# Kernel tuning notes

Hardware: AMD Instinct MI355X
Metric: run time of the kernel (lower is better)

Reference implementation:

```python
import jax, jax.numpy as jnp
import numpy as np
from jax import lax

C_IN, C_KEY, C_VAL = 1024, 256, 512

def conv3x3(x, w, b):
    # x: [B,C_in,H,W], w: [C_out,C_in,3,3] -> SAME padding, stride 1
    y = lax.conv_general_dilated(x, w, window_strides=(1, 1), padding='SAME',
                                 dimension_numbers=('NCHW', 'OIHW', 'NCHW'))
    return y + b[None, :, None, None]

def setup_inputs() -> dict:
    key = jax.random.key(0)
    ks = jax.random.split(key, 10)
    B, H, W = 16, 32, 32
    conv_std = 0.01  # matches torch init.normal_(std=0.01)
    inp = {
        'src_temp': jax.random.normal(ks[0], (B, C_IN, H, W), jnp.float32),
        'src_search': jax.random.normal(ks[1], (B, C_IN, H, W), jnp.float32),
        'wk_m': jax.random.normal(ks[2], (C_KEY, C_IN, 3, 3), jnp.float32) * conv_std,
        'bk_m': jnp.zeros((C_KEY,), jnp.float32),
        'wv_m': jax.random.normal(ks[3], (C_VAL, C_IN, 3, 3), jnp.float32) * conv_std,
        'bv_m': jnp.zeros((C_VAL,), jnp.float32),
        'wk_q': jax.random.normal(ks[4], (C_KEY, C_IN, 3, 3), jnp.float32) * conv_std,
        'bk_q': jnp.zeros((C_KEY,), jnp.float32),
        'wv_q': jax.random.normal(ks[5], (C_VAL, C_IN, 3, 3), jnp.float32) * conv_std,
        'bv_q': jnp.zeros((C_VAL,), jnp.float32),
    }
    return inp

def reference(src_temp, src_search, wk_m, bk_m, wv_m, bv_m, wk_q, bk_q, wv_q, bv_q):
    # key/value projections
    m_key = conv3x3(src_temp, wk_m, bk_m)      # [B, Ck, H, W]
    m_value = conv3x3(src_temp, wv_m, bv_m)    # [B, Cv, H, W]
    q_key = conv3x3(src_search, wk_q, bk_q)    # [B, Ck, H, W]
    q_value = conv3x3(src_search, wv_q, bv_q)  # [B, Cv, H, W]

    B, Ck, H, W = m_key.shape
    Cv = m_value.shape[1]
    HW = H * W

    mk = m_key.reshape(B, Ck, HW)   # [B, Ck, HW_m]
    qk = q_key.reshape(B, Ck, HW)   # [B, Ck, HW_q]
    # scores: [B, HW_m, HW_q]
    w = jnp.einsum('bcm,bcq->bmq', mk, qk) / jnp.sqrt(jnp.float32(Ck))
    w = jax.nn.softmax(w, axis=1)   # normalize over memory locations

    mv = m_value.reshape(B, Cv, HW)            # [B, Cv, HW_m]
    mem_info = jnp.einsum('bcm,bmq->bcq', mv, w).reshape(B, Cv, H, W)
    return jnp.concatenate([mem_info, q_value], axis=1)  # [B, 2*Cv, H, W]
```

## Files before the change

### kernel.cpp

```cpp
#include <hip/hip_runtime.h>
#include <stdint.h>

typedef __bf16 bf16;
typedef __bf16 bf16x8 __attribute__((ext_vector_type(8)));
typedef float  f32x4  __attribute__((ext_vector_type(4)));
typedef unsigned int u32;

#define OFF_A16HI 0ull
#define OFF_A16LO 37879808ull
#define OFF_A8HI  0ull
#define OFF_A8LO  18939904ull
#define OFF_W1HI  75759616ull
#define OFF_W1LO  89915392ull
#define OFF_W0HI  37879808ull
#define OFF_W0LO  52035584ull
#define OFF_MKEYT 67108864ull
#define OFF_MVAL  83886080ull
#define OFF_QKEYT 117440512ull
#define OFF_WATTN 0ull

__device__ __forceinline__ void split(float v, bf16& h, bf16& l) {
    h = (bf16)v;
    l = (bf16)(v - (float)h);
}

__device__ __forceinline__ u32 packsplit(float v) {
    bf16 h = (bf16)v;
    bf16 l = (bf16)(v - (float)h);
    unsigned short hu = __builtin_bit_cast(unsigned short, h);
    unsigned short lu = __builtin_bit_cast(unsigned short, l);
    return (u32)hu | ((u32)lu << 16);
}

__device__ __forceinline__ void deint4(const uint4 v, uint2& h, uint2& l) {
    h.x = (v.x & 0xffffu) | (v.y << 16);
    h.y = (v.z & 0xffffu) | (v.w << 16);
    l.x = (v.x >> 16) | (v.y & 0xffff0000u);
    l.y = (v.z >> 16) | (v.w & 0xffff0000u);
}

__global__ __launch_bounds__(256) void k_wt(const float* __restrict__ wk,
                                            const float* __restrict__ wv,
                                            bf16* __restrict__ Wh, bf16* __restrict__ Wl) {
    size_t id = (size_t)blockIdx.x * 256 + threadIdx.x;
    int e = (int)(id & 7);
    size_t t = id >> 3;
    int mm = (int)(t % 96); t /= 96;
    int coff = (int)(t & 3); t >>= 2;
    int cch = (int)(t & 31); t >>= 5;
    int r = (int)(t % 9);
    int mt = (int)(t / 9);
    int m = mt * 96 + mm;
    int c = cch * 32 + coff * 8 + e;
    float v = (m < 256) ? wk[((size_t)m * 1024 + c) * 9 + r]
                        : wv[((size_t)(m - 256) * 1024 + c) * 9 + r];
    bf16 h, l;
    split(v, h, l);
    Wh[id] = h; Wl[id] = l;
}

__global__ __launch_bounds__(256) void k_zero(bf16* __restrict__ A) {
    int id = blockIdx.x * 256 + threadIdx.x;
    int oct = id & 127;
    int t = id >> 7;
    int pos = t % 132; t /= 132;
    int yy, xx;
    if (pos < 34)       { yy = 0;  xx = pos; }
    else if (pos < 68)  { yy = 33; xx = pos - 34; }
    else if (pos < 100) { yy = pos - 68 + 1;  xx = 0; }
    else                { yy = pos - 100 + 1; xx = 33; }
    size_t off = (((size_t)t * 1156) + yy * 34 + xx) * 1024 + (size_t)oct * 8;
    *(uint4*)(A + off) = make_uint4(0u, 0u, 0u, 0u);
}

__global__ __launch_bounds__(256) void k_transpose(const float* __restrict__ src,
                                                   bf16* __restrict__ Ah, bf16* __restrict__ Al) {
    int pt = blockIdx.x, ct = blockIdx.y, bl = blockIdx.z;
    __shared__ float tile[64][68];
    int t = threadIdx.x;
    #pragma unroll
    for (int k = 0; k < 4; ++k) {
        int idx = t + 256 * k;
        int c = idx >> 4, f4 = idx & 15;
        float4 v = *(const float4*)(src + ((size_t)bl * 1024 + ct * 64 + c) * 1024 + pt * 64 + f4 * 4);
        *(float4*)&tile[c][f4 * 4] = v;
    }
    __syncthreads();
    #pragma unroll
    for (int k = 0; k < 2; ++k) {
        int s = t + 256 * k;
        int px = s >> 3, oct = s & 7;
        bf16x8 vh, vl;
        #pragma unroll
        for (int e = 0; e < 8; ++e) {
            bf16 h, l;
            split(tile[oct * 8 + e][px], h, l);
            vh[e] = h; vl[e] = l;
        }
        int pxg = pt * 64 + px;
        int yy = (pxg >> 5) + 1, xx = (pxg & 31) + 1;
        size_t off = (((size_t)bl * 34 + yy) * 34 + xx) * 1024 + ct * 64 + oct * 8;
        *(bf16x8*)(Ah + off) = vh;
        *(bf16x8*)(Al + off) = vl;
    }
}

#define XS_STRIDE 40

#define XS_H6 (6 * 34 * XS_STRIDE)
__global__ __launch_bounds__(256) void k_conv16(const bf16* __restrict__ Ah, const bf16* __restrict__ Al,
                                                const bf16* __restrict__ Wh, const bf16* __restrict__ Wl,
                                                const float* __restrict__ biask, const float* __restrict__ biasv,
                                                u32* __restrict__ keyT, float* __restrict__ valf) {
    int id = blockIdx.x;
    int mt = id & 7;
    int r2 = id >> 3;
    int bl = r2 >> 3;
    int rg = r2 & 7;
    int y0 = rg * 4;
    int b = bl;

    __shared__ bf16 Xs[2 * XS_H6];

    int tid = threadIdx.x;
    int w = tid >> 6, l = tid & 63;
    int wm = (w & 1) * 48, wn = (w >> 1) * 64;
    int lm = l & 15, lq = l >> 4;
    int koff = lq * 8;

    f32x4 acc[3][4] = {};

    const size_t Abase = ((size_t)bl * 34 + y0) * 34 * 1024;
    const size_t wlane = (size_t)lq * 768 + (size_t)lm * 8;

    const bf16* gsrc[7];
    int lidx[7];
    #pragma unroll
    for (int it = 0; it < 7; ++it) {
        int s = tid + 256 * it;
        if (s < 1632) {
            int hl = s >= 816;
            int r816 = s - hl * 816;
            int row = r816 / 136;
            int rr = r816 - row * 136;
            int px = rr >> 2, oct = rr & 3;
            const bf16* base = hl ? Al : Ah;
            gsrc[it] = base + Abase + ((size_t)row * 34 + px) * 1024 + oct * 8;
            lidx[it] = ((hl * 6 + row) * 34 + px) * XS_STRIDE + oct * 8;
        } else { gsrc[it] = nullptr; lidx[it] = -1; }
    }

    for (int cch = 0; cch < 32; ++cch) {
        int c0 = cch * 32;
        bf16x8 xv[7];
        #pragma unroll
        for (int it = 0; it < 7; ++it)
            if (lidx[it] >= 0) xv[it] = *(const bf16x8*)(gsrc[it] + c0);
        __syncthreads();
        #pragma unroll
        for (int it = 0; it < 7; ++it)
            if (lidx[it] >= 0) *(bf16x8*)&Xs[lidx[it]] = xv[it];
        __syncthreads();

        #pragma unroll
        for (int r = 0; r < 9; ++r) {
            int dy = r / 3, dx = r % 3;
            size_t wblk = (((size_t)mt * 9 + r) * 32 + cch) * 3072 + wlane;
            bf16x8 ah[3], al[3];
            #pragma unroll
            for (int i = 0; i < 3; ++i) {
                size_t o = wblk + (size_t)(wm + i * 16) * 8;
                ah[i] = *(const bf16x8*)(Wh + o);
                al[i] = *(const bf16x8*)(Wl + o);
            }
            #pragma unroll
            for (int j = 0; j < 4; ++j) {
                int n = wn + j * 16 + lm;
                int lbase = (((n >> 5) + dy) * 34 + (n & 31) + dx) * XS_STRIDE + koff;
                bf16x8 bh  = *(const bf16x8*)&Xs[lbase];
                bf16x8 blo = *(const bf16x8*)&Xs[XS_H6 + lbase];
                #pragma unroll
                for (int i = 0; i < 3; ++i) {
                    acc[i][j] = __builtin_amdgcn_mfma_f32_16x16x32_bf16(ah[i], bh,  acc[i][j], 0, 0, 0);
                    acc[i][j] = __builtin_amdgcn_mfma_f32_16x16x32_bf16(ah[i], blo, acc[i][j], 0, 0, 0);
                    acc[i][j] = __builtin_amdgcn_mfma_f32_16x16x32_bf16(al[i], bh,  acc[i][j], 0, 0, 0);
                }
            }
        }
    }

    int col = lm, rowb = lq * 4;
    #pragma unroll
    for (int i = 0; i < 3; ++i) {
        int ch4 = mt * 96 + wm + i * 16 + rowb;
        #pragma unroll
        for (int j = 0; j < 4; ++j) {
            int px = rg * 128 + wn + j * 16 + col;
            if (ch4 < 256) {
                u32 p0 = packsplit(acc[i][j][0] + biask[ch4 + 0]);
                u32 p1 = packsplit(acc[i][j][1] + biask[ch4 + 1]);
                u32 p2 = packsplit(acc[i][j][2] + biask[ch4 + 2]);
                u32 p3 = packsplit(acc[i][j][3] + biask[ch4 + 3]);
                *(uint4*)(keyT + ((size_t)b * 1024 + px) * 256 + ch4) = make_uint4(p0, p1, p2, p3);
            } else {
                int cv = ch4 - 256;
                #pragma unroll
                for (int e = 0; e < 4; ++e)
                    valf[((size_t)b * 1024 + 512 + cv + e) * 1024 + px] = acc[i][j][e] + biasv[cv + e];
            }
        }
    }
}

#define XS_H4 (4 * 34 * XS_STRIDE)
__global__ __launch_bounds__(256) void k_conv8(const bf16* __restrict__ Ah, const bf16* __restrict__ Al,
                                               const bf16* __restrict__ Wh, const bf16* __restrict__ Wl,
                                               const float* __restrict__ biask, const float* __restrict__ biasv,
                                               u32* __restrict__ keyT, u32* __restrict__ valp, int bglob) {
    int id = blockIdx.x;
    int mt = id & 7;
    int r2 = id >> 3;
    int bl = r2 >> 4;
    int rg = r2 & 15;
    int y0 = rg * 2;
    int b = bglob + bl;

    __shared__ bf16 Xs[2 * XS_H4];

    int tid = threadIdx.x;
    int w = tid >> 6, l = tid & 63;
    int wm = (w & 1) * 48, wn = (w >> 1) * 32;
    int lm = l & 15, lq = l >> 4;
    int koff = lq * 8;

    f32x4 acc[3][2] = {};

    const size_t Abase = ((size_t)bl * 34 + y0) * 34 * 1024;
    const size_t wlane = (size_t)lq * 768 + (size_t)lm * 8;

    const bf16* gsrc[5];
    int lidx[5];
    #pragma unroll
    for (int it = 0; it < 5; ++it) {
        int s = tid + 256 * it;
        if (s < 1088) {
            int hl = s >= 544;
            int r544 = s - hl * 544;
            int row = r544 / 136;
            int rr = r544 - row * 136;
            int px = rr >> 2, oct = rr & 3;
            const bf16* base = hl ? Al : Ah;
            gsrc[it] = base + Abase + ((size_t)row * 34 + px) * 1024 + oct * 8;
            lidx[it] = ((hl * 4 + row) * 34 + px) * XS_STRIDE + oct * 8;
        } else { gsrc[it] = nullptr; lidx[it] = -1; }
    }

    for (int cch = 0; cch < 32; ++cch) {
        int c0 = cch * 32;
        bf16x8 xv[5];
        #pragma unroll
        for (int it = 0; it < 5; ++it)
            if (lidx[it] >= 0) xv[it] = *(const bf16x8*)(gsrc[it] + c0);
        __syncthreads();
        #pragma unroll
        for (int it = 0; it < 5; ++it)
            if (lidx[it] >= 0) *(bf16x8*)&Xs[lidx[it]] = xv[it];
        __syncthreads();

        #pragma unroll
        for (int r = 0; r < 9; ++r) {
            int dy = r / 3, dx = r % 3;
            size_t wblk = (((size_t)mt * 9 + r) * 32 + cch) * 3072 + wlane;
            bf16x8 ah[3], al[3];
            #pragma unroll
            for (int i = 0; i < 3; ++i) {
                size_t o = wblk + (size_t)(wm + i * 16) * 8;
                ah[i] = *(const bf16x8*)(Wh + o);
                al[i] = *(const bf16x8*)(Wl + o);
            }
            #pragma unroll
            for (int j = 0; j < 2; ++j) {
                int n = wn + j * 16 + lm;
                int lbase = (((n >> 5) + dy) * 34 + (n & 31) + dx) * XS_STRIDE + koff;
                bf16x8 bh  = *(const bf16x8*)&Xs[lbase];
                bf16x8 blo = *(const bf16x8*)&Xs[XS_H4 + lbase];
                #pragma unroll
                for (int i = 0; i < 3; ++i) {
                    acc[i][j] = __builtin_amdgcn_mfma_f32_16x16x32_bf16(ah[i], bh,  acc[i][j], 0, 0, 0);
                    acc[i][j] = __builtin_amdgcn_mfma_f32_16x16x32_bf16(ah[i], blo, acc[i][j], 0, 0, 0);
                    acc[i][j] = __builtin_amdgcn_mfma_f32_16x16x32_bf16(al[i], bh,  acc[i][j], 0, 0, 0);
                }
            }
        }
    }

    int col = lm, rowb = lq * 4;
    #pragma unroll
    for (int i = 0; i < 3; ++i) {
        int ch4 = mt * 96 + wm + i * 16 + rowb;
        #pragma unroll
        for (int j = 0; j < 2; ++j) {
            int px = rg * 64 + wn + j * 16 + col;
            if (ch4 < 256) {
                u32 p0 = packsplit(acc[i][j][0] + biask[ch4 + 0]);
                u32 p1 = packsplit(acc[i][j][1] + biask[ch4 + 1]);
                u32 p2 = packsplit(acc[i][j][2] + biask[ch4 + 2]);
                u32 p3 = packsplit(acc[i][j][3] + biask[ch4 + 3]);
                *(uint4*)(keyT + ((size_t)b * 1024 + px) * 256 + ch4) = make_uint4(p0, p1, p2, p3);
            } else {
                int cv = ch4 - 256;
                #pragma unroll
                for (int e = 0; e < 4; ++e)
                    valp[((size_t)b * 512 + cv + e) * 1024 + px] = packsplit(acc[i][j][e] + biasv[cv + e]);
            }
        }
    }
}

#define AS 40
__global__ __launch_bounds__(256) void k_scores(const u32* __restrict__ qkT,
                                                const u32* __restrict__ mkT,
                                                float* __restrict__ wattn) {
    int mt = blockIdx.x, qt = blockIdx.y, b = blockIdx.z;
    __shared__ bf16 Qh[128][AS], Ql[128][AS], Mh[128][AS], Ml[128][AS];
    int t = threadIdx.x;
    int w_ = t >> 6, l = t & 63;
    int wq = (w_ & 1) * 64, wm = (w_ >> 1) * 64;
    int lm = l & 15, lq = l >> 4, koff = lq * 8;
    int srow = t >> 1, sc4 = (t & 1) * 16;
    const u32* qbase = qkT + ((size_t)b * 1024 + qt * 128 + srow) * 256 + sc4;
    const u32* mbase = mkT + ((size_t)b * 1024 + mt * 128 + srow) * 256 + sc4;
    f32x4 acc[4][4] = {};
    uint4 qv[4], mv[4];
    #pragma unroll
    for (int k = 0; k < 4; ++k) { qv[k] = *(const uint4*)(qbase + k * 4); mv[k] = *(const uint4*)(mbase + k * 4); }
    for (int cc = 0; cc < 8; ++cc) {
        __syncthreads();
        #pragma unroll
        for (int k = 0; k < 4; ++k) {
            uint2 h, lo;
            deint4(qv[k], h, lo);
            *(uint2*)&Qh[srow][sc4 + k * 4] = h;
            *(uint2*)&Ql[srow][sc4 + k * 4] = lo;
            deint4(mv[k], h, lo);
            *(uint2*)&Mh[srow][sc4 + k * 4] = h;
            *(uint2*)&Ml[srow][sc4 + k * 4] = lo;
        }
        __syncthreads();
        if (cc < 7) {
            #pragma unroll
            for (int k = 0; k < 4; ++k) {
                qv[k] = *(const uint4*)(qbase + (cc + 1) * 32 + k * 4);
                mv[k] = *(const uint4*)(mbase + (cc + 1) * 32 + k * 4);
            }
        }
        bf16x8 ah[4], al[4];
        #pragma unroll
        for (int iq = 0; iq < 4; ++iq) {
            ah[iq] = *(const bf16x8*)&Qh[wq + iq * 16 + lm][koff];
            al[iq] = *(const bf16x8*)&Ql[wq + iq * 16 + lm][koff];
        }
        #pragma unroll
        for (int jm = 0; jm < 4; ++jm) {
            bf16x8 bh = *(const bf16x8*)&Mh[wm + jm * 16 + lm][koff];
            bf16x8 bl = *(const bf16x8*)&Ml[wm + jm * 16 + lm][koff];
            #pragma unroll
            for (int iq = 0; iq < 4; ++iq) {
                acc[iq][jm] = __builtin_amdgcn_mfma_f32_16x16x32_bf16(ah[iq], bh, acc[iq][jm], 0, 0, 0);
                acc[iq][jm] = __builtin_amdgcn_mfma_f32_16x16x32_bf16(ah[iq], bl, acc[iq][jm], 0, 0, 0);
                acc[iq][jm] = __builtin_amdgcn_mfma_f32_16x16x32_bf16(al[iq], bh, acc[iq][jm], 0, 0, 0);
            }
        }
    }
    #pragma unroll
    for (int iq = 0; iq < 4; ++iq) {
        int q = qt * 128 + wq + iq * 16 + lq * 4;
        #pragma unroll
        for (int jm = 0; jm < 4; ++jm) {
            int m = mt * 128 + wm + jm * 16 + lm;
            float* wp = wattn + ((size_t)b * 1024 + q) * 1024 + m;
            #pragma unroll
            for (int e = 0; e < 4; ++e)
                wp[(size_t)e * 1024] = acc[iq][jm][e] * 0.0625f;
        }
    }
}

__global__ __launch_bounds__(256) void k_softmax(float* __restrict__ wattn) {
    int row = blockIdx.x * 4 + (threadIdx.x >> 6);
    int l = threadIdx.x & 63;
    float* base = wattn + (size_t)row * 1024;
    float4 v[4];
    #pragma unroll
    for (int k = 0; k < 4; ++k) v[k] = *(float4*)(base + l * 4 + k * 256);
    float f[16];
    #pragma unroll
    for (int k = 0; k < 4; ++k) { f[4*k]=v[k].x; f[4*k+1]=v[k].y; f[4*k+2]=v[k].z; f[4*k+3]=v[k].w; }
    float mx = -3.0e38f;
    #pragma unroll
    for (int e = 0; e < 16; ++e) mx = fmaxf(mx, f[e]);
    #pragma unroll
    for (int off = 32; off > 0; off >>= 1) mx = fmaxf(mx, __shfl_xor(mx, off));
    float s = 0.0f;
    #pragma unroll
    for (int e = 0; e < 16; ++e) { f[e] = __expf(f[e] - mx); s += f[e]; }
    #pragma unroll
    for (int off = 32; off > 0; off >>= 1) s += __shfl_xor(s, off);
    float inv = 1.0f / s;
    u32* ub = (u32*)base;
    #pragma unroll
    for (int k = 0; k < 4; ++k) {
        uint4 u = make_uint4(packsplit(f[4*k]   * inv), packsplit(f[4*k+1] * inv),
                             packsplit(f[4*k+2] * inv), packsplit(f[4*k+3] * inv));
        *(uint4*)(ub + l * 4 + k * 256) = u;
    }
}

__global__ __launch_bounds__(256) void k_memv(const u32* __restrict__ mvalp,
                                              const u32* __restrict__ wattnp,
                                              float* __restrict__ outp) {
    int ct = blockIdx.x, qt = blockIdx.y, b = blockIdx.z;
    __shared__ bf16 Vh[128][AS], Vl[128][AS], Wh[128][AS], Wl[128][AS];
    int t = threadIdx.x;
    int w_ = t >> 6, l = t & 63;
    int wc = (w_ & 1) * 64, wq = (w_ >> 1) * 64;
    int lm = l & 15, lq = l >> 4, koff = lq * 8;
    int srow = t >> 1, sc4 = (t & 1) * 16;
    const u32* vbase = mvalp  + ((size_t)b * 512  + ct * 128 + srow) * 1024 + sc4;
    const u32* wbase = wattnp + ((size_t)b * 1024 + qt * 128 + srow) * 1024 + sc4;
    f32x4 acc[4][4] = {};
    uint4 vv[4], wv[4];
    #pragma unroll
    for (int k = 0; k < 4; ++k) { vv[k] = *(const uint4*)(vbase + k * 4); wv[k] = *(const uint4*)(wbase + k * 4); }
    for (int mc = 0; mc < 32; ++mc) {
        __syncthreads();
        #pragma unroll
        for (int k = 0; k < 4; ++k) {
            uint2 h, lo;
            deint4(vv[k], h, lo);
            *(uint2*)&Vh[srow][sc4 + k * 4] = h;
            *(uint2*)&Vl[srow][sc4 + k * 4] = lo;
            deint4(wv[k], h, lo);
            *(uint2*)&Wh[srow][sc4 + k * 4] = h;
            *(uint2*)&Wl[srow][sc4 + k * 4] = lo;
        }
        __syncthreads();
        if (mc < 31) {
            #pragma unroll
            for (int k = 0; k < 4; ++k) {
                vv[k] = *(const uint4*)(vbase + (mc + 1) * 32 + k * 4);
                wv[k] = *(const uint4*)(wbase + (mc + 1) * 32 + k * 4);
            }
        }
        bf16x8 ah[4], al[4];
        #pragma unroll
        for (int ic = 0; ic < 4; ++ic) {
            ah[ic] = *(const bf16x8*)&Vh[wc + ic * 16 + lm][koff];
            al[ic] = *(const bf16x8*)&Vl[wc + ic * 16 + lm][koff];
        }
        #pragma unroll
        for (int jq = 0; jq < 4; ++jq) {
            bf16x8 bh = *(const bf16x8*)&Wh[wq + jq * 16 + lm][koff];
            bf16x8 bl = *(const bf16x8*)&Wl[wq + jq * 16 + lm][koff];
            #pragma unroll
            for (int ic = 0; ic < 4; ++ic) {
                acc[ic][jq] = __builtin_amdgcn_mfma_f32_16x16x32_bf16(ah[ic], bh, acc[ic][jq], 0, 0, 0);
                acc[ic][jq] = __builtin_amdgcn_mfma_f32_16x16x32_bf16(ah[ic], bl, acc[ic][jq], 0, 0, 0);
                acc[ic][jq] = __builtin_amdgcn_mfma_f32_16x16x32_bf16(al[ic], bh, acc[ic][jq], 0, 0, 0);
            }
        }
    }
    #pragma unroll
    for (int ic = 0; ic < 4; ++ic) {
        int c = ct * 128 + wc + ic * 16 + lq * 4;
        #pragma unroll
        for (int jq = 0; jq < 4; ++jq) {
            int q = qt * 128 + wq + jq * 16 + lm;
            #pragma unroll
            for (int e = 0; e < 4; ++e)
                outp[((size_t)b * 1024 + c + e) * 1024 + q] = acc[ic][jq][e];
        }
    }
}

extern "C" void kernel_launch(void* const* d_in, const int* in_sizes, int n_in,
                              void* d_out, int out_size, void* d_ws, size_t ws_size,
                              hipStream_t stream) {
    const float* src_temp   = (const float*)d_in[0];
    const float* src_search = (const float*)d_in[1];
    const float* wk_m = (const float*)d_in[2];
    const float* bk_m = (const float*)d_in[3];
    const float* wv_m = (const float*)d_in[4];
    const float* bv_m = (const float*)d_in[5];
    const float* wk_q = (const float*)d_in[6];
    const float* bk_q = (const float*)d_in[7];
    const float* wv_q = (const float*)d_in[8];
    const float* bv_q = (const float*)d_in[9];
    float* out = (float*)d_out;
    char* ws = (char*)d_ws;

    bf16* A    = (bf16*)(ws + OFF_A16HI);
    bf16* Ah16 = (bf16*)(ws + OFF_A16HI);
    bf16* Al16 = (bf16*)(ws + OFF_A16LO);
    bf16* Ah8  = (bf16*)(ws + OFF_A8HI);
    bf16* Al8  = (bf16*)(ws + OFF_A8LO);
    bf16* W1h  = (bf16*)(ws + OFF_W1HI);
    bf16* W1l  = (bf16*)(ws + OFF_W1LO);
    bf16* W0h  = (bf16*)(ws + OFF_W0HI);
    bf16* W0l  = (bf16*)(ws + OFF_W0LO);
    u32* qkP   = (u32*)(ws + OFF_QKEYT);
    u32* mkP   = (u32*)(ws + OFF_MKEYT);
    u32* mvP   = (u32*)(ws + OFF_MVAL);
    float* wattn = (float*)(ws + OFF_WATTN);
    u32* wattnP  = (u32*)(ws + OFF_WATTN);

    hipLaunchKernelGGL(k_zero, dim3(2112), dim3(256), 0, stream, A);

    hipLaunchKernelGGL(k_wt, dim3(27648), dim3(256), 0, stream, wk_q, wv_q, W1h, W1l);
    hipLaunchKernelGGL(k_transpose, dim3(16, 16, 16), dim3(256), 0, stream,
                       src_search, Ah16, Al16);
    hipLaunchKernelGGL(k_conv16, dim3(1024), dim3(256), 0, stream,
                       Ah16, Al16, W1h, W1l, bk_q, bv_q, qkP, out);

    hipLaunchKernelGGL(k_wt, dim3(27648), dim3(256), 0, stream, wk_m, wv_m, W0h, W0l);
    for (int h = 0; h < 2; ++h) {
        hipLaunchKernelGGL(k_transpose, dim3(16, 16, 8), dim3(256), 0, stream,
                           src_temp + (size_t)h * 8 * 1024 * 1024, Ah8, Al8);
        hipLaunchKernelGGL(k_conv8, dim3(1024), dim3(256), 0, stream,
                           Ah8, Al8, W0h, W0l, bk_m, bv_m, mkP, mvP, h * 8);
    }

    hipLaunchKernelGGL(k_scores,  dim3(8, 8, 16), dim3(256), 0, stream, qkP, mkP, wattn);
    hipLaunchKernelGGL(k_softmax, dim3(4096),     dim3(256), 0, stream, wattn);
    hipLaunchKernelGGL(k_memv,    dim3(4, 8, 16), dim3(256), 0, stream, mvP, wattnP, out);
}
```

Baseline: 1.636 ms.

## Load conv input tiles directly into LDS with XOR-swizzled interleaved hi/lo layout

After: 1.531 ms. -6.4%, faster.

```diff
diff --git a/kernel.cpp b/kernel.cpp
--- a/kernel.cpp
+++ b/kernel.cpp
@@ -37,6 +37,13 @@
     h.y = (v.z & 0xffffu) | (v.w << 16);
     l.x = (v.x >> 16) | (v.y & 0xffff0000u);
     l.y = (v.z >> 16) | (v.w & 0xffff0000u);
+}
+
+__device__ __forceinline__ void gl_lds16(const bf16* g, bf16* l) {
+    __builtin_amdgcn_global_load_lds(
+        (const __attribute__((address_space(1))) void*)g,
+        (__attribute__((address_space(3))) void*)l,
+        16, 0, 0);
 }
 
 __global__ __launch_bounds__(256) void k_wt(const float* __restrict__ wk,
@@ -105,9 +112,7 @@
     }
 }
 
-#define XS_STRIDE 40
-
-#define XS_H6 (6 * 34 * XS_STRIDE)
+
 __global__ __launch_bounds__(256) void k_conv16(const bf16* __restrict__ Ah, const bf16* __restrict__ Al,
                                                 const bf16* __restrict__ Wh, const bf16* __restrict__ Wl,
                                                 const float* __restrict__ biask, const float* __restrict__ biasv,
@@ -120,13 +125,12 @@
     int y0 = rg * 4;
     int b = bl;
 
-    __shared__ bf16 Xs[2 * XS_H6];
+    __shared__ bf16 Xs[6 * 34 * 64];
 
     int tid = threadIdx.x;
     int w = tid >> 6, l = tid & 63;
     int wm = (w & 1) * 48, wn = (w >> 1) * 64;
     int lm = l & 15, lq = l >> 4;
-    int koff = lq * 8;
 
     f32x4 acc[3][4] = {};
 
@@ -134,32 +138,25 @@
     const size_t wlane = (size_t)lq * 768 + (size_t)lm * 8;
 
     const bf16* gsrc[7];
-    int lidx[7];
     #pragma unroll
     for (int it = 0; it < 7; ++it) {
         int s = tid + 256 * it;
         if (s < 1632) {
-            int hl = s >= 816;
-            int r816 = s - hl * 816;
-            int row = r816 / 136;
-            int rr = r816 - row * 136;
-            int px = rr >> 2, oct = rr & 3;
-            const bf16* base = hl ? Al : Ah;
-            gsrc[it] = base + Abase + ((size_t)row * 34 + px) * 1024 + oct * 8;
-            lidx[it] = ((hl * 6 + row) * 34 + px) * XS_STRIDE + oct * 8;
-        } else { gsrc[it] = nullptr; lidx[it] = -1; }
+            int row = s / 272;
+            int rem = s - row * 272;
+            int px = rem >> 3, j = rem & 7;
+            int hlk = j ^ (px & 7);
+            const bf16* base = (hlk & 4) ? Al : Ah;
+            gsrc[it] = base + Abase + ((size_t)row * 34 + px) * 1024 + (hlk & 3) * 8;
+        } else gsrc[it] = nullptr;
     }
 
     for (int cch = 0; cch < 32; ++cch) {
         int c0 = cch * 32;
-        bf16x8 xv[7];
+        __syncthreads();
         #pragma unroll
         for (int it = 0; it < 7; ++it)
-            if (lidx[it] >= 0) xv[it] = *(const bf16x8*)(gsrc[it] + c0);
-        __syncthreads();
-        #pragma unroll
-        for (int it = 0; it < 7; ++it)
-            if (lidx[it] >= 0) *(bf16x8*)&Xs[lidx[it]] = xv[it];
+            if (gsrc[it]) gl_lds16(gsrc[it] + c0, &Xs[2048 * it + 512 * w]);
         __syncthreads();
 
         #pragma unroll
@@ -176,9 +173,11 @@
             #pragma unroll
             for (int j = 0; j < 4; ++j) {
                 int n = wn + j * 16 + lm;
-                int lbase = (((n >> 5) + dy) * 34 + (n & 31) + dx) * XS_STRIDE + koff;
-                bf16x8 bh  = *(const bf16x8*)&Xs[lbase];
-                bf16x8 blo = *(const bf16x8*)&Xs[XS_H6 + lbase];
+                int px = (n & 31) + dx;
+                int row = (n >> 5) + dy;
+                int eb = ((row * 34 + px) << 6) + ((lq ^ (px & 7)) << 3);
+                bf16x8 bh  = *(const bf16x8*)&Xs[eb];
+                bf16x8 blo = *(const bf16x8*)&Xs[eb ^ 32];
                 #pragma unroll
                 for (int i = 0; i < 3; ++i) {
                     acc[i][j] = __builtin_amdgcn_mfma_f32_16x16x32_bf16(ah[i], bh,  acc[i][j], 0, 0, 0);
@@ -212,7 +211,6 @@
     }
 }
 
-#define XS_H4 (4 * 34 * XS_STRIDE)
 __global__ __launch_bounds__(256) void k_conv8(const bf16* __restrict__ Ah, const bf16* __restrict__ Al,
                                                const bf16* __restrict__ Wh, const bf16* __restrict__ Wl,
                                                const float* __restrict__ biask, const float* __restrict__ biasv,
@@ -225,13 +223,12 @@
     int y0 = rg * 2;
     int b = bglob + bl;
 
-    __shared__ bf16 Xs[2 * XS_H4];
+    __shared__ bf16 Xs[4 * 34 * 64];
 
     int tid = threadIdx.x;
     int w = tid >> 6, l = tid & 63;
     int wm = (w & 1) * 48, wn = (w >> 1) * 32;
     int lm = l & 15, lq = l >> 4;
-    int koff = lq * 8;
 
     f32x4 acc[3][2] = {};
 
@@ -239,32 +236,25 @@
     const size_t wlane = (size_t)lq * 768 + (size_t)lm * 8;
 
     const bf16* gsrc[5];
-    int lidx[5];
     #pragma unroll
     for (int it = 0; it < 5; ++it) {
         int s = tid + 256 * it;
         if (s < 1088) {
-            int hl = s >= 544;
-            int r544 = s - hl * 544;
-            int row = r544 / 136;
-            int rr = r544 - row * 136;
-            int px = rr >> 2, oct = rr & 3;
-            const bf16* base = hl ? Al : Ah;
-            gsrc[it] = base + Abase + ((size_t)row * 34 + px) * 1024 + oct * 8;
-            lidx[it] = ((hl * 4 + row) * 34 + px) * XS_STRIDE + oct * 8;
-        } else { gsrc[it] = nullptr; lidx[it] = -1; }
+            int row = s / 272;
+            int rem = s - row * 272;
+            int px = rem >> 3, j = rem & 7;
+            int hlk = j ^ (px & 7);
+            const bf16* base = (hlk & 4) ? Al : Ah;
+            gsrc[it] = base + Abase + ((size_t)row * 34 + px) * 1024 + (hlk & 3) * 8;
+        } else gsrc[it] = nullptr;
     }
 
     for (int cch = 0; cch < 32; ++cch) {
         int c0 = cch * 32;
-        bf16x8 xv[5];
+        __syncthreads();
         #pragma unroll
         for (int it = 0; it < 5; ++it)
-            if (lidx[it] >= 0) xv[it] = *(const bf16x8*)(gsrc[it] + c0);
-        __syncthreads();
-        #pragma unroll
-        for (int it = 0; it < 5; ++it)
-            if (lidx[it] >= 0) *(bf16x8*)&Xs[lidx[it]] = xv[it];
+            if (gsrc[it]) gl_lds16(gsrc[it] + c0, &Xs[2048 * it + 512 * w]);
         __syncthreads();
 
         #pragma unroll
@@ -281,9 +271,11 @@
             #pragma unroll
             for (int j = 0; j < 2; ++j) {
                 int n = wn + j * 16 + lm;
-                int lbase = (((n >> 5) + dy) * 34 + (n & 31) + dx) * XS_STRIDE + koff;
-                bf16x8 bh  = *(const bf16x8*)&Xs[lbase];
-                bf16x8 blo = *(const bf16x8*)&Xs[XS_H4 + lbase];
+                int px = (n & 31) + dx;
+                int row = (n >> 5) + dy;
+                int eb = ((row * 34 + px) << 6) + ((lq ^ (px & 7)) << 3);
+                bf16x8 bh  = *(const bf16x8*)&Xs[eb];
+                bf16x8 blo = *(const bf16x8*)&Xs[eb ^ 32];
                 #pragma unroll
                 for (int i = 0; i < 3; ++i) {
                     acc[i][j] = __builtin_amdgcn_mfma_f32_16x16x32_bf16(ah[i], bh,  acc[i][j], 0, 0, 0);
```
